# Performance work log

Measured on AMD Instinct MI355X. Metric: run time of the kernel, lower is better.

Reference implementation:

```python
import jax, jax.numpy as jnp
import numpy as np

EPS = 1e-5

def _layernorm(x, w, b):
    mu = jnp.mean(x, axis=-1, keepdims=True)
    var = jnp.var(x, axis=-1, keepdims=True)
    return (x - mu) * jax.lax.rsqrt(var + EPS) * w + b

def setup_inputs() -> dict:
    key = jax.random.key(0)
    ks = jax.random.split(key, 8)
    B, N, D = 1, 512, 128
    s = 1.0 / np.sqrt(D)
    return {
        "z": jax.random.normal(ks[0], (B, N, N, D), jnp.float32),
        "mask": jnp.ones((B, N, N), jnp.float32),
        "norm_in_w": jnp.ones((D,), jnp.float32),
        "norm_in_b": jnp.zeros((D,), jnp.float32),
        "wp": jax.random.normal(ks[1], (2 * D, D), jnp.float32) * s,  # linear_p.weight
        "wg": jax.random.normal(ks[2], (2 * D, D), jnp.float32) * s,  # linear_g.weight
        "norm_out_w": jnp.ones((D,), jnp.float32),
        "norm_out_b": jnp.zeros((D,), jnp.float32),
        "w_out": jax.random.normal(ks[3], (D, D), jnp.float32) * s,   # output_projection.weight
        "w_gate": jax.random.normal(ks[4], (D, D), jnp.float32) * s,  # output_gate.weight (zero-init in module; random here so grads are nontrivial)
    }

def reference(z, mask, norm_in_w, norm_in_b, wp, wg, norm_out_w, norm_out_b, w_out, w_gate):
    # z: (B,N,N,D), mask: (B,N,N)
    h = _layernorm(z, norm_in_w, norm_in_b)                    # (B,N,N,D)
    p = jnp.einsum('bijd,ed->bije', h, wp)                      # (B,N,N,2D)
    g = jax.nn.sigmoid(jnp.einsum('bijd,ed->bije', h, wg))     # (B,N,N,2D)
    ab = p * g * mask[..., None]
    a, b = jnp.split(ab, 2, axis=-1)                            # each (B,N,N,D)
    # outgoing: x_ij = sum_k a_ik * b_jk
    x = jnp.einsum('bikd,bjkd->bijd', a, b)
    x = _layernorm(x, norm_out_w, norm_out_b)
    out = jnp.einsum('bijd,ed->bije', x, w_out)
    gate = jax.nn.sigmoid(jnp.einsum('bijd,ed->bije', h, w_gate))
    return out * gate
```

## Files before the change

kernel.cpp:

```cpp
#include <hip/hip_runtime.h>
#include <cstdint>

#define NDIM 512
#define DDIM 128
#define NN (512 * 512)

typedef unsigned short u16;
typedef short bf16x8 __attribute__((ext_vector_type(8)));
typedef float f32x4 __attribute__((ext_vector_type(4)));

union I4U { int4 v; u16 s[8]; };

__device__ __forceinline__ u16 f2bf(float f) {
  unsigned u = __builtin_bit_cast(unsigned, f);
  u += 0x7fffu + ((u >> 16) & 1u);
  return (u16)(u >> 16);
}
__device__ __forceinline__ float bf2f(u16 s) {
  return __builtin_bit_cast(float, ((unsigned)s) << 16);
}
__device__ __forceinline__ float sigm(float x) {
  return 1.0f / (1.0f + __expf(-x));
}
__device__ __forceinline__ unsigned cvtpk(float lo, float hi) {
  unsigned r;
  asm("v_cvt_pk_bf16_f32 %0, %1, %2" : "=v"(r) : "v"(lo), "v"(hi));
  return r;
}
__device__ __forceinline__ void gload16(void* lds_base, const void* gsrc) {
  __builtin_amdgcn_global_load_lds((const __attribute__((address_space(1))) void*)gsrc,
                                   (__attribute__((address_space(3))) void*)lds_base,
                                   16, 0, 0);
}

__global__ __launch_bounds__(256) void k_prep(const float* __restrict__ wp,
                                              const float* __restrict__ wg,
                                              const float* __restrict__ wga,
                                              const float* __restrict__ wo,
                                              u16* __restrict__ Wbig, u16* __restrict__ Wout) {
  int i = blockIdx.x * 256 + threadIdx.x;
  if (i < 640 * 128) {
    int r = i >> 7, c = i & 127;
    float v = (r < 256) ? wp[r * 128 + c] : (r < 512) ? wg[(r - 256) * 128 + c]
                                                      : wga[(r - 512) * 128 + c];
    Wbig[i] = f2bf(v);
  } else {
    int j = i - 640 * 128;
    Wout[j] = f2bf(wo[j]);
  }
}

__global__ __launch_bounds__(512, 4) void k_pass1(
    const float* __restrict__ z, const float* __restrict__ mask,
    const float* __restrict__ niw, const float* __restrict__ nib,
    const u16* __restrict__ Wbig,
    u16* __restrict__ a_t, u16* __restrict__ b_t, u16* __restrict__ gate) {
  __shared__ __align__(16) char lds[81920];
  const int t = threadIdx.x;
  const int ij0 = blockIdx.x * 64;
  const int wv = t >> 6, l = t & 63;

  auto stage_chunk = [&](int c) {
    char* wb = lds + 16384 + (c & 1) * 16384;
#pragma unroll
    for (int r = 0; r < 2; ++r) {
      const int o = r * 8192 + t * 16;
      const int rowIT = (o >> 8) & 15;
      const int colb = o & 255;
      const int tsel = (o >> 12);
      int tile;
      if (c < 8) tile = ((c & 1) << 4) + ((c >> 1) << 2) + tsel;
      else       tile = 32 + ((c - 8) << 1) + (tsel & 1) + ((tsel >> 1) << 2);
      const char* src = (const char*)Wbig + tile * 4096 + rowIT * 256 +
                        (colb ^ ((rowIT & 7) << 4));
      gload16(wb + r * 8192 + wv * 1024, src);
    }
  };

  stage_chunk(0);

  {
    const int row = t >> 3, seg = t & 7;
    const float4* zp = (const float4*)(z + (size_t)(ij0 + row) * 128 + seg * 16);
    float zv[16];
    {
      float4 a0 = zp[0], a1 = zp[1], a2 = zp[2], a3 = zp[3];
      zv[0]=a0.x; zv[1]=a0.y; zv[2]=a0.z; zv[3]=a0.w;
      zv[4]=a1.x; zv[5]=a1.y; zv[6]=a1.z; zv[7]=a1.w;
      zv[8]=a2.x; zv[9]=a2.y; zv[10]=a2.z; zv[11]=a2.w;
      zv[12]=a3.x; zv[13]=a3.y; zv[14]=a3.z; zv[15]=a3.w;
    }
    float s = 0.f, ss = 0.f;
#pragma unroll
    for (int j = 0; j < 16; j++) { s += zv[j]; ss += zv[j] * zv[j]; }
    s += __shfl_xor(s, 1); s += __shfl_xor(s, 2); s += __shfl_xor(s, 4);
    ss += __shfl_xor(ss, 1); ss += __shfl_xor(ss, 2); ss += __shfl_xor(ss, 4);
    const float mu = s * (1.f / 128.f);
    const float var = ss * (1.f / 128.f) - mu * mu;
    const float rs = rsqrtf(var + 1e-5f);
    float wv_[16], bv_[16];
    {
      const float4* wq = (const float4*)(niw + seg * 16);
      const float4* bq = (const float4*)(nib + seg * 16);
      float4 w0=wq[0],w1=wq[1],w2=wq[2],w3=wq[3], b0=bq[0],b1=bq[1],b2=bq[2],b3=bq[3];
      wv_[0]=w0.x;wv_[1]=w0.y;wv_[2]=w0.z;wv_[3]=w0.w; wv_[4]=w1.x;wv_[5]=w1.y;wv_[6]=w1.z;wv_[7]=w1.w;
      wv_[8]=w2.x;wv_[9]=w2.y;wv_[10]=w2.z;wv_[11]=w2.w; wv_[12]=w3.x;wv_[13]=w3.y;wv_[14]=w3.z;wv_[15]=w3.w;
      bv_[0]=b0.x;bv_[1]=b0.y;bv_[2]=b0.z;bv_[3]=b0.w; bv_[4]=b1.x;bv_[5]=b1.y;bv_[6]=b1.z;bv_[7]=b1.w;
      bv_[8]=b2.x;bv_[9]=b2.y;bv_[10]=b2.z;bv_[11]=b2.w; bv_[12]=b3.x;bv_[13]=b3.y;bv_[14]=b3.z;bv_[15]=b3.w;
    }
    I4U p0, p1;
#pragma unroll
    for (int j = 0; j < 4; j++) {
      unsigned w = cvtpk((zv[2*j] - mu) * rs * wv_[2*j] + bv_[2*j],
                         (zv[2*j+1] - mu) * rs * wv_[2*j+1] + bv_[2*j+1]);
      p0.s[2*j] = (u16)(w & 0xffff); p0.s[2*j+1] = (u16)(w >> 16);
    }
#pragma unroll
    for (int j = 0; j < 4; j++) {
      unsigned w = cvtpk((zv[8+2*j] - mu) * rs * wv_[8+2*j] + bv_[8+2*j],
                         (zv[9+2*j] - mu) * rs * wv_[9+2*j] + bv_[9+2*j]);
      p1.s[2*j] = (u16)(w & 0xffff); p1.s[2*j+1] = (u16)(w >> 16);
    }
    char* base = lds + row * 256;
    const int sw = (row & 7) << 4;
    *(int4*)(base + ((seg * 32) ^ sw)) = p0.v;
    *(int4*)(base + ((seg * 32 + 16) ^ sw)) = p1.v;
  }
  __syncthreads();

  const int wr = wv & 3, wc = wv >> 2;
  const int l15 = l & 15, l4 = l >> 4;

  const int arow = wr * 16 + l15;
  const char* abase = lds + arow * 256;
  const int asw = (arow & 7) << 4;
  bf16x8 af[4];
#pragma unroll
  for (int ks = 0; ks < 4; ks++)
    af[ks] = *(const bf16x8*)(abase + ((ks * 64 + l4 * 16) ^ asw));

  const int ijl = wr * 16 + l4 * 4;
  float mk[4];
#pragma unroll
  for (int r = 0; r < 4; r++) mk[r] = mask[ij0 + ijl + r];

  char* ab = lds + 49152;
  const int sw15 = (l15 & 7) << 4;
  f32x4 ap[2];

#pragma unroll
  for (int c = 0; c < 10; ++c) {
    if (c < 9) stage_chunk(c + 1);
    const char* wb = lds + 16384 + (c & 1) * 16384;
    if (c < 8 && (c & 1) == 0) {
#pragma unroll
      for (int s = 0; s < 2; ++s) {
        ap[s] = (f32x4){0.f, 0.f, 0.f, 0.f};
#pragma unroll
        for (int ks = 0; ks < 4; ++ks) {
          bf16x8 b = *(const bf16x8*)(wb + (2 * wc + s) * 4096 + l15 * 256 +
                                      ((ks * 64 + l4 * 16) ^ sw15));
          ap[s] = __builtin_amdgcn_mfma_f32_16x16x32_bf16(af[ks], b, ap[s], 0, 0, 0);
        }
      }
    } else if (c < 8) {
      const int q = c >> 1;
#pragma unroll
      for (int s = 0; s < 2; ++s) {
        f32x4 ag = (f32x4){0.f, 0.f, 0.f, 0.f};
#pragma unroll
        for (int ks = 0; ks < 4; ++ks) {
          bf16x8 b = *(const bf16x8*)(wb + (2 * wc + s) * 4096 + l15 * 256 +
                                      ((ks * 64 + l4 * 16) ^ sw15));
          ag = __builtin_amdgcn_mfma_f32_16x16x32_bf16(af[ks], b, ag, 0, 0, 0);
        }
        const int cl = 32 * wc + s * 16 + l15;
        unsigned w0 = cvtpk(ap[s][0] * sigm(ag[0]) * mk[0],
                            ap[s][1] * sigm(ag[1]) * mk[1]);
        unsigned w1 = cvtpk(ap[s][2] * sigm(ag[2]) * mk[2],
                            ap[s][3] * sigm(ag[3]) * mk[3]);
        unsigned long long uu = (unsigned long long)w0 | ((unsigned long long)w1 << 32);
        *(unsigned long long*)(ab + q * 8192 + cl * 128 + ((ijl * 2) ^ ((cl & 7) << 4))) = uu;
      }
    } else {
      if (c == 8) {
        const int col = t >> 3, seg = t & 7;
        const int swc = (col & 7) << 4;
#pragma unroll
        for (int qq = 0; qq < 4; ++qq) {
          int4 v = *(const int4*)(ab + qq * 8192 + col * 128 + ((seg * 16) ^ swc));
          u16* dst = (qq < 2 ? a_t : b_t) + (size_t)((qq & 1) * 64 + col) * NN + ij0 + seg * 8;
          *(int4*)dst = v;
        }
      }
      const int cbase = (c == 8) ? 0 : 32;
#pragma unroll
      for (int s = 0; s < 2; ++s) {
        f32x4 ag = (f32x4){0.f, 0.f, 0.f, 0.f};
#pragma unroll
        for (int ks = 0; ks < 4; ++ks) {
          bf16x8 b = *(const bf16x8*)(wb + (2 * wc + s) * 4096 + l15 * 256 +
                                      ((ks * 64 + l4 * 16) ^ sw15));
          ag = __builtin_amdgcn_mfma_f32_16x16x32_bf16(af[ks], b, ag, 0, 0, 0);
        }
        const int col2 = 2 * (cbase + wc * 64 + s * 16 + l15);
        unsigned w0 = cvtpk(sigm(ag[0]), sigm(ag[1]));
        unsigned w1 = cvtpk(sigm(ag[2]), sigm(ag[3]));
        *(u16*)(lds + (ijl + 0) * 256 + (col2 ^ (((ijl + 0) & 7) << 4))) = (u16)(w0 & 0xffff);
        *(u16*)(lds + (ijl + 1) * 256 + (col2 ^ (((ijl + 1) & 7) << 4))) = (u16)(w0 >> 16);
        *(u16*)(lds + (ijl + 2) * 256 + (col2 ^ (((ijl + 2) & 7) << 4))) = (u16)(w1 & 0xffff);
        *(u16*)(lds + (ijl + 3) * 256 + (col2 ^ (((ijl + 3) & 7) << 4))) = (u16)(w1 >> 16);
      }
    }
    __syncthreads();
  }

  {
    const int row = t >> 3, seg = t & 7;
    const int sw = (row & 7) << 4;
    int4 v0 = *(const int4*)(lds + row * 256 + ((seg * 32) ^ sw));
    int4 v1 = *(const int4*)(lds + row * 256 + ((seg * 32 + 16) ^ sw));
    u16* gdst = gate + (size_t)(ij0 + row) * 128 + seg * 16;
    ((int4*)gdst)[0] = v0;
    ((int4*)gdst)[1] = v1;
  }
}

__global__ __launch_bounds__(256) void k_pass2(const u16* __restrict__ a_t,
                                               const u16* __restrict__ b_t,
                                               u16* __restrict__ x_t) {
  __shared__ __align__(16) char lds[32768];
  const int b2 = ((int)blockIdx.x & 7) * 256 + ((int)blockIdx.x >> 3);
  const int d = b2 >> 4;
  const int tile = b2 & 15;
  const int row0 = (tile >> 2) * 128, col0 = (tile & 3) * 128;
  const char* A = (const char*)(a_t + (size_t)d * NN);
  const char* B = (const char*)(b_t + (size_t)d * NN);
  const int t = threadIdx.x;
  const int wv = t >> 6, l = t & 63;
  const int wr = wv >> 1, wc = wv & 1;
  const int l15 = l & 15, l4 = l >> 4;
  char* al = lds;
  char* bl = lds + 16384;
  f32x4 acc[4][4];
#pragma unroll
  for (int m = 0; m < 4; m++)
#pragma unroll
    for (int n = 0; n < 4; n++) acc[m][n] = (f32x4){0.f, 0.f, 0.f, 0.f};

  for (int ks = 0; ks < 8; ks++) {
#pragma unroll
    for (int it = 0; it < 4; it++) {
      const int f = it * 256 + t;
      const int row = f >> 3, kc = f & 7;
      const int ldsoff = (it * 256 + wv * 64) * 16;
      gload16(al + ldsoff, A + (size_t)(row0 + row) * 1024 + ks * 128 + kc * 16);
      gload16(bl + ldsoff, B + (size_t)(col0 + row) * 1024 + ks * 128 + kc * 16);
    }
    __syncthreads();
#pragma unroll
    for (int kk = 0; kk < 2; kk++) {
      bf16x8 af[4], bfr[4];
#pragma unroll
      for (int m = 0; m < 4; m++)
        af[m] = *(const bf16x8*)(al + (wr * 64 + m * 16 + l15) * 128 + kk * 64 + l4 * 16);
#pragma unroll
      for (int n = 0; n < 4; n++)
        bfr[n] = *(const bf16x8*)(bl + (wc * 64 + n * 16 + l15) * 128 + kk * 64 + l4 * 16);
#pragma unroll
      for (int m = 0; m < 4; m++)
#pragma unroll
        for (int n = 0; n < 4; n++)
          acc[m][n] = __builtin_amdgcn_mfma_f32_16x16x32_bf16(af[m], bfr[n], acc[m][n], 0, 0, 0);
    }
    __syncthreads();
  }
#pragma unroll
  for (int m = 0; m < 4; m++) {
#pragma unroll
    for (int r = 0; r < 4; r++) {
      const int row = wr * 64 + m * 16 + l4 * 4 + r;
      const int sw = (row & 7) << 4;
      char* rowp = lds + row * 256;
#pragma unroll
      for (int n = 0; n < 4; n++) {
        const int col = wc * 64 + n * 16 + l15;
        *(short*)(rowp + ((col * 2) ^ sw)) = (short)f2bf(acc[m][n][r]);
      }
    }
  }
  __syncthreads();
  {
    const int row = t >> 1, q = t & 1;
    const int sw = (row & 7) << 4;
    const char* rowp = lds + row * 256;
    int4 v[8];
#pragma unroll
    for (int c = 0; c < 8; c++)
      v[c] = *(const int4*)(rowp + ((q * 128 + c * 16) ^ sw));
    u16* dst = x_t + (size_t)d * NN + (size_t)(row0 + row) * 512 + col0 + q * 64;
#pragma unroll
    for (int c = 0; c < 8; c++) ((int4*)dst)[c] = v[c];
  }
}

__global__ __launch_bounds__(256) void k_pass3(const u16* __restrict__ x_t,
                                               const u16* __restrict__ gate,
                                               const float* __restrict__ now_,
                                               const float* __restrict__ nob,
                                               const u16* __restrict__ Wout,
                                               float* __restrict__ out) {
  __shared__ __align__(16) char xl[16384];
  const int t = threadIdx.x;
  const int ij0 = blockIdx.x * 64;
  {
    const int d = t >> 1, q = t & 1;
    const int4* src = (const int4*)(x_t + (size_t)d * NN + ij0 + q * 32);
#pragma unroll
    for (int c = 0; c < 4; c++) {
      I4U v; v.v = src[c];
#pragma unroll
      for (int j = 0; j < 8; j++) {
        const int ij = q * 32 + c * 8 + j;
        *(short*)(xl + ij * 256 + ((2 * d) ^ ((ij & 7) << 4))) = (short)v.s[j];
      }
    }
  }
  __syncthreads();
  {
    const int row = t >> 2, seg = t & 3;
    char* base = xl + row * 256;
    const int sw = (row & 7) << 4;
    float f[32];
#pragma unroll
    for (int c = 0; c < 4; c++) {
      I4U v; v.v = *(const int4*)(base + ((seg * 64 + c * 16) ^ sw));
#pragma unroll
      for (int j = 0; j < 8; j++) f[c * 8 + j] = bf2f(v.s[j]);
    }
    float s = 0.f, ss = 0.f;
#pragma unroll
    for (int j = 0; j < 32; j++) { s += f[j]; ss += f[j] * f[j]; }
    s += __shfl_xor(s, 1); s += __shfl_xor(s, 2);
    ss += __shfl_xor(ss, 1); ss += __shfl_xor(ss, 2);
    const float mu = s * (1.f / 128.f);
    const float var = ss * (1.f / 128.f) - mu * mu;
    const float rs = rsqrtf(var + 1e-5f);
#pragma unroll
    for (int c = 0; c < 4; c++) {
      const float4 w0 = *(const float4*)(now_ + seg * 32 + c * 8);
      const float4 w1 = *(const float4*)(now_ + seg * 32 + c * 8 + 4);
      const float4 b0 = *(const float4*)(nob + seg * 32 + c * 8);
      const float4 b1 = *(const float4*)(nob + seg * 32 + c * 8 + 4);
      I4U o;
      o.s[0] = f2bf((f[c*8+0] - mu) * rs * w0.x + b0.x);
      o.s[1] = f2bf((f[c*8+1] - mu) * rs * w0.y + b0.y);
      o.s[2] = f2bf((f[c*8+2] - mu) * rs * w0.z + b0.z);
      o.s[3] = f2bf((f[c*8+3] - mu) * rs * w0.w + b0.w);
      o.s[4] = f2bf((f[c*8+4] - mu) * rs * w1.x + b1.x);
      o.s[5] = f2bf((f[c*8+5] - mu) * rs * w1.y + b1.y);
      o.s[6] = f2bf((f[c*8+6] - mu) * rs * w1.z + b1.z);
      o.s[7] = f2bf((f[c*8+7] - mu) * rs * w1.w + b1.w);
      *(int4*)(base + ((seg * 64 + c * 16) ^ sw)) = o.v;
    }
  }
  __syncthreads();
  const int wv = t >> 6, l = t & 63;
  const int l15 = l & 15, l4 = l >> 4;
  const int arow = wv * 16 + l15;
  const char* abase = xl + arow * 256;
  const int asw = (arow & 7) << 4;
  const char* wbase = (const char*)Wout + l15 * 256 + l4 * 16;
  f32x4 acc[8];
#pragma unroll
  for (int n = 0; n < 8; n++) acc[n] = (f32x4){0.f, 0.f, 0.f, 0.f};
#pragma unroll
  for (int ks = 0; ks < 4; ks++) {
    bf16x8 af = *(const bf16x8*)(abase + ((ks * 64 + l4 * 16) ^ asw));
#pragma unroll
    for (int n = 0; n < 8; n++) {
      bf16x8 bfr = *(const bf16x8*)(wbase + n * 4096 + ks * 64);
      acc[n] = __builtin_amdgcn_mfma_f32_16x16x32_bf16(af, bfr, acc[n], 0, 0, 0);
    }
  }
  const int rowb = wv * 16 + (l4 << 2);
#pragma unroll
  for (int n = 0; n < 8; n++) {
    const int e = n * 16 + l15;
#pragma unroll
    for (int r = 0; r < 4; r++) {
      const size_t idx = (size_t)(ij0 + rowb + r) * 128 + e;
      out[idx] = acc[n][r] * bf2f(gate[idx]);
    }
  }
}

extern "C" void kernel_launch(void* const* d_in, const int* in_sizes, int n_in,
                              void* d_out, int out_size, void* d_ws, size_t ws_size,
                              hipStream_t stream) {
  const float* z    = (const float*)d_in[0];
  const float* mask = (const float*)d_in[1];
  const float* niw  = (const float*)d_in[2];
  const float* nib  = (const float*)d_in[3];
  const float* wp   = (const float*)d_in[4];
  const float* wg   = (const float*)d_in[5];
  const float* now_ = (const float*)d_in[6];
  const float* nob  = (const float*)d_in[7];
  const float* wo   = (const float*)d_in[8];
  const float* wga  = (const float*)d_in[9];
  float* out = (float*)d_out;
  char* ws = (char*)d_ws;

  u16* Wbig = (u16*)ws;
  u16* Wout = (u16*)(ws + 0x28000);
  u16* a_t  = (u16*)(ws + 0x100000);
  u16* b_t  = (u16*)(ws + 0x100000 + 0x4000000);
  u16* x_t  = (u16*)(ws + 0x100000 + 0x8000000);
  u16* gate = (u16*)(ws + 0x100000 + 0xC000000);

  hipLaunchKernelGGL(k_prep, dim3(384), dim3(256), 0, stream, wp, wg, wga, wo, Wbig, Wout);
  hipLaunchKernelGGL(k_pass1, dim3(4096), dim3(512), 0, stream, z, mask, niw, nib, Wbig, a_t, b_t, gate);
  hipLaunchKernelGGL(k_pass2, dim3(2048), dim3(256), 0, stream, a_t, b_t, x_t);
  hipLaunchKernelGGL(k_pass3, dim3(4096), dim3(256), 0, stream, x_t, gate, now_, nob, Wout, out);
  (void)in_sizes; (void)n_in; (void)out_size; (void)ws_size;
}
```

Measured before the change: 506.8 us.

## Write pass1 outputs directly to global in transposed layout, stage Wout in LDS

Pass1 now writes a/b and the gate directly from MFMA accumulators to global memory as 8-byte transposed stores. This drops the LDS staging buffers and the final copy-out, shrinking shared memory from 80KB to 48KB, which could raise occupancy. The gate is stored transposed (feature-major), so pass3 reads it with 8-byte loads per output column. Pass3 also stages Wout into swizzled LDS via async loads, repacks x_t with wider loads and vector LDS stores, and uses packed bf16 conversion; the risk is less coalesced 8-byte global stores in pass1.

New measurement: 476.5 us. 6.0% less time.

```diff
diff --git a/kernel.cpp b/kernel.cpp
--- a/kernel.cpp
+++ b/kernel.cpp
@@ -8,6 +8,7 @@
 typedef unsigned short u16;
 typedef short bf16x8 __attribute__((ext_vector_type(8)));
 typedef float f32x4 __attribute__((ext_vector_type(4)));
+typedef unsigned long long u64;
 
 union I4U { int4 v; u16 s[8]; };
 
@@ -54,8 +55,8 @@
     const float* __restrict__ z, const float* __restrict__ mask,
     const float* __restrict__ niw, const float* __restrict__ nib,
     const u16* __restrict__ Wbig,
-    u16* __restrict__ a_t, u16* __restrict__ b_t, u16* __restrict__ gate) {
-  __shared__ __align__(16) char lds[81920];
+    u16* __restrict__ a_t, u16* __restrict__ b_t, u16* __restrict__ gate_t) {
+  __shared__ __align__(16) char lds[49152];
   const int t = threadIdx.x;
   const int ij0 = blockIdx.x * 64;
   const int wv = t >> 6, l = t & 63;
@@ -144,7 +145,6 @@
 #pragma unroll
   for (int r = 0; r < 4; r++) mk[r] = mask[ij0 + ijl + r];
 
-  char* ab = lds + 49152;
   const int sw15 = (l15 & 7) << 4;
   f32x4 ap[2];
 
@@ -174,25 +174,17 @@
                                       ((ks * 64 + l4 * 16) ^ sw15));
           ag = __builtin_amdgcn_mfma_f32_16x16x32_bf16(af[ks], b, ag, 0, 0, 0);
         }
-        const int cl = 32 * wc + s * 16 + l15;
+        const int e = q * 64 + 32 * wc + s * 16 + l15;
         unsigned w0 = cvtpk(ap[s][0] * sigm(ag[0]) * mk[0],
                             ap[s][1] * sigm(ag[1]) * mk[1]);
         unsigned w1 = cvtpk(ap[s][2] * sigm(ag[2]) * mk[2],
                             ap[s][3] * sigm(ag[3]) * mk[3]);
-        unsigned long long uu = (unsigned long long)w0 | ((unsigned long long)w1 << 32);
-        *(unsigned long long*)(ab + q * 8192 + cl * 128 + ((ijl * 2) ^ ((cl & 7) << 4))) = uu;
+        u64 uu = (u64)w0 | ((u64)w1 << 32);
+        u16* dst = (e < 128 ? a_t + (size_t)e * NN
+                            : b_t + (size_t)(e - 128) * NN) + ij0 + ijl;
+        *(u64*)dst = uu;
       }
     } else {
-      if (c == 8) {
-        const int col = t >> 3, seg = t & 7;
-        const int swc = (col & 7) << 4;
-#pragma unroll
-        for (int qq = 0; qq < 4; ++qq) {
-          int4 v = *(const int4*)(ab + qq * 8192 + col * 128 + ((seg * 16) ^ swc));
-          u16* dst = (qq < 2 ? a_t : b_t) + (size_t)((qq & 1) * 64 + col) * NN + ij0 + seg * 8;
-          *(int4*)dst = v;
-        }
-      }
       const int cbase = (c == 8) ? 0 : 32;
 #pragma unroll
       for (int s = 0; s < 2; ++s) {
@@ -203,26 +195,14 @@
                                       ((ks * 64 + l4 * 16) ^ sw15));
           ag = __builtin_amdgcn_mfma_f32_16x16x32_bf16(af[ks], b, ag, 0, 0, 0);
         }
-        const int col2 = 2 * (cbase + wc * 64 + s * 16 + l15);
+        const int col = cbase + wc * 64 + s * 16 + l15;
         unsigned w0 = cvtpk(sigm(ag[0]), sigm(ag[1]));
         unsigned w1 = cvtpk(sigm(ag[2]), sigm(ag[3]));
-        *(u16*)(lds + (ijl + 0) * 256 + (col2 ^ (((ijl + 0) & 7) << 4))) = (u16)(w0 & 0xffff);
-        *(u16*)(lds + (ijl + 1) * 256 + (col2 ^ (((ijl + 1) & 7) << 4))) = (u16)(w0 >> 16);
-        *(u16*)(lds + (ijl + 2) * 256 + (col2 ^ (((ijl + 2) & 7) << 4))) = (u16)(w1 & 0xffff);
-        *(u16*)(lds + (ijl + 3) * 256 + (col2 ^ (((ijl + 3) & 7) << 4))) = (u16)(w1 >> 16);
+        u64 uu = (u64)w0 | ((u64)w1 << 32);
+        *(u64*)(gate_t + (size_t)col * NN + ij0 + ijl) = uu;
       }
     }
     __syncthreads();
-  }
-
-  {
-    const int row = t >> 3, seg = t & 7;
-    const int sw = (row & 7) << 4;
-    int4 v0 = *(const int4*)(lds + row * 256 + ((seg * 32) ^ sw));
-    int4 v1 = *(const int4*)(lds + row * 256 + ((seg * 32 + 16) ^ sw));
-    u16* gdst = gate + (size_t)(ij0 + row) * 128 + seg * 16;
-    ((int4*)gdst)[0] = v0;
-    ((int4*)gdst)[1] = v1;
   }
 }
 
@@ -305,28 +285,42 @@
 }
 
 __global__ __launch_bounds__(256) void k_pass3(const u16* __restrict__ x_t,
-                                               const u16* __restrict__ gate,
+                                               const u16* __restrict__ gate_t,
                                                const float* __restrict__ now_,
                                                const float* __restrict__ nob,
                                                const u16* __restrict__ Wout,
                                                float* __restrict__ out) {
   __shared__ __align__(16) char xl[16384];
+  __shared__ __align__(16) char wl[32768];
   const int t = threadIdx.x;
   const int ij0 = blockIdx.x * 64;
+  const int wv = t >> 6;
+
+#pragma unroll
+  for (int r = 0; r < 8; ++r) {
+    const int off = r * 4096 + t * 16;
+    const int row = off >> 8, col = off & 255;
+    gload16(wl + r * 4096 + wv * 1024,
+            (const char*)Wout + row * 256 + (col ^ ((row & 7) << 4)));
+  }
+
   {
-    const int d = t >> 1, q = t & 1;
-    const int4* src = (const int4*)(x_t + (size_t)d * NN + ij0 + q * 32);
-#pragma unroll
-    for (int c = 0; c < 4; c++) {
-      I4U v; v.v = src[c];
-#pragma unroll
-      for (int j = 0; j < 8; j++) {
-        const int ij = q * 32 + c * 8 + j;
-        *(short*)(xl + ij * 256 + ((2 * d) ^ ((ij & 7) << 4))) = (short)v.s[j];
-      }
+    const int iq = t & 15, o = t >> 4;
+    u64 rk[8];
+#pragma unroll
+    for (int k = 0; k < 8; ++k)
+      rk[k] = *(const u64*)(x_t + (size_t)(o * 8 + k) * NN + ij0 + iq * 4);
+#pragma unroll
+    for (int i = 0; i < 4; ++i) {
+      I4U ov;
+#pragma unroll
+      for (int k = 0; k < 8; ++k) ov.s[k] = (u16)(rk[k] >> (16 * i));
+      const int ij = iq * 4 + i;
+      *(int4*)(xl + ij * 256 + ((o * 16) ^ ((ij & 7) << 4))) = ov.v;
     }
   }
   __syncthreads();
+
   {
     const int row = t >> 2, seg = t & 3;
     char* base = xl + row * 256;
@@ -353,24 +347,28 @@
       const float4 b0 = *(const float4*)(nob + seg * 32 + c * 8);
       const float4 b1 = *(const float4*)(nob + seg * 32 + c * 8 + 4);
       I4U o;
-      o.s[0] = f2bf((f[c*8+0] - mu) * rs * w0.x + b0.x);
-      o.s[1] = f2bf((f[c*8+1] - mu) * rs * w0.y + b0.y);
-      o.s[2] = f2bf((f[c*8+2] - mu) * rs * w0.z + b0.z);
-      o.s[3] = f2bf((f[c*8+3] - mu) * rs * w0.w + b0.w);
-      o.s[4] = f2bf((f[c*8+4] - mu) * rs * w1.x + b1.x);
-      o.s[5] = f2bf((f[c*8+5] - mu) * rs * w1.y + b1.y);
-      o.s[6] = f2bf((f[c*8+6] - mu) * rs * w1.z + b1.z);
-      o.s[7] = f2bf((f[c*8+7] - mu) * rs * w1.w + b1.w);
+      unsigned q0 = cvtpk((f[c*8+0] - mu) * rs * w0.x + b0.x,
+                          (f[c*8+1] - mu) * rs * w0.y + b0.y);
+      unsigned q1 = cvtpk((f[c*8+2] - mu) * rs * w0.z + b0.z,
+                          (f[c*8+3] - mu) * rs * w0.w + b0.w);
+      unsigned q2 = cvtpk((f[c*8+4] - mu) * rs * w1.x + b1.x,
+                          (f[c*8+5] - mu) * rs * w1.y + b1.y);
+      unsigned q3 = cvtpk((f[c*8+6] - mu) * rs * w1.z + b1.z,
+                          (f[c*8+7] - mu) * rs * w1.w + b1.w);
+      o.s[0]=(u16)(q0&0xffff); o.s[1]=(u16)(q0>>16);
+      o.s[2]=(u16)(q1&0xffff); o.s[3]=(u16)(q1>>16);
+      o.s[4]=(u16)(q2&0xffff); o.s[5]=(u16)(q2>>16);
+      o.s[6]=(u16)(q3&0xffff); o.s[7]=(u16)(q3>>16);
       *(int4*)(base + ((seg * 64 + c * 16) ^ sw)) = o.v;
     }
   }
   __syncthreads();
-  const int wv = t >> 6, l = t & 63;
+
+  const int l = t & 63;
   const int l15 = l & 15, l4 = l >> 4;
   const int arow = wv * 16 + l15;
   const char* abase = xl + arow * 256;
   const int asw = (arow & 7) << 4;
-  const char* wbase = (const char*)Wout + l15 * 256 + l4 * 16;
   f32x4 acc[8];
 #pragma unroll
   for (int n = 0; n < 8; n++) acc[n] = (f32x4){0.f, 0.f, 0.f, 0.f};
@@ -379,7 +377,9 @@
     bf16x8 af = *(const bf16x8*)(abase + ((ks * 64 + l4 * 16) ^ asw));
 #pragma unroll
     for (int n = 0; n < 8; n++) {
-      bf16x8 bfr = *(const bf16x8*)(wbase + n * 4096 + ks * 64);
+      const int erow = n * 16 + l15;
+      bf16x8 bfr = *(const bf16x8*)(wl + erow * 256 +
+                                    ((ks * 64 + l4 * 16) ^ ((erow & 7) << 4)));
       acc[n] = __builtin_amdgcn_mfma_f32_16x16x32_bf16(af, bfr, acc[n], 0, 0, 0);
     }
   }
@@ -387,10 +387,11 @@
 #pragma unroll
   for (int n = 0; n < 8; n++) {
     const int e = n * 16 + l15;
+    const u64 g4 = *(const u64*)(gate_t + (size_t)e * NN + ij0 + rowb);
 #pragma unroll
     for (int r = 0; r < 4; r++) {
       const size_t idx = (size_t)(ij0 + rowb + r) * 128 + e;
-      out[idx] = acc[n][r] * bf2f(gate[idx]);
+      out[idx] = acc[n][r] * bf2f((u16)(g4 >> (16 * r)));
     }
   }
 }
```
